# Kernel optimization log

Measured on AMD Instinct MI355X. Metric: run time of the kernel, lower is better.

## Reference

```python
import jax, jax.numpy as jnp
import numpy as np

D_MODEL = 128
N_HEADS = 8
D_K = D_MODEL // N_HEADS
N_NODES = 50000
N_EDGES = 800000


def setup_inputs() -> dict:
    key = jax.random.key(0)
    ks = jax.random.split(key, 8)
    X = jax.random.normal(ks[0], (N_NODES, D_MODEL), dtype=jnp.float32)
    nbr_src = jax.random.randint(ks[1], (N_EDGES,), 0, N_NODES, dtype=jnp.int32)
    nbr_dst = jax.random.randint(ks[2], (N_EDGES,), 0, N_NODES, dtype=jnp.int32)
    s = 1.0 / np.sqrt(D_MODEL)
    W_qkv = jax.random.normal(ks[3], (3 * D_MODEL, D_MODEL), dtype=jnp.float32) * s
    w_bias = jax.random.normal(ks[4], (N_HEADS, D_MODEL), dtype=jnp.float32) * s
    W_gate = jax.random.normal(ks[5], (D_MODEL, D_MODEL), dtype=jnp.float32) * s
    b_gate = jax.random.normal(ks[6], (D_MODEL,), dtype=jnp.float32) * s
    W_o = jax.random.normal(ks[7], (D_MODEL, D_MODEL), dtype=jnp.float32) * s
    return {"X": X, "W_qkv": W_qkv, "w_bias": w_bias, "W_gate": W_gate,
            "b_gate": b_gate, "W_o": W_o, "nbr_src": nbr_src,
            "nbr_dst": nbr_dst, "num_cells": N_NODES}


def segment_softmax(scores, seg, num_segments):
    # scores: [E, H], seg: [E] -> softmax over edges sharing the same seg id
    mx = jax.ops.segment_max(scores, seg, num_segments=num_segments)  # [N, H]
    mx = jnp.where(jnp.isfinite(mx), mx, -1e9)
    exp_s = jnp.exp(scores - mx[seg])
    sm = jax.ops.segment_sum(exp_s, seg, num_segments=num_segments)  # [N, H]
    return exp_s / (sm[seg] + 1e-12)


def reference(X, W_qkv, w_bias, W_gate, b_gate, W_o, nbr_src, nbr_dst, num_cells):
    H, dk = N_HEADS, D_K
    scale = 1.0 / np.sqrt(dk)
    qkv = (X @ W_qkv.T).reshape(-1, 3, H, dk)      # [N, 3, H, dk]
    Q, K, V = qkv[:, 0], qkv[:, 1], qkv[:, 2]
    gate = jax.nn.sigmoid(X @ W_gate.T + b_gate).reshape(-1, H, dk)
    bias = X @ w_bias.T                             # [N, H]
    scores = jnp.einsum('ehd,ehd->eh', Q[nbr_src], K[nbr_dst]) * scale + bias[nbr_src]
    attn = segment_softmax(scores, nbr_src, num_cells)          # [E, H]
    out = jax.ops.segment_sum(attn[:, :, None] * V[nbr_dst], nbr_src,
                              num_segments=num_cells)           # [N, H, dk]
    return (gate * out).reshape(-1, D_MODEL) @ W_o.T
```

## Files before the change

### kernel.cpp

```cpp
#include <hip/hip_runtime.h>
#include <hip/hip_fp16.h>

#define DM 128
#define NHEADS 8
#define MAXDEG 64
#define SROW 136

typedef _Float16 half8 __attribute__((ext_vector_type(8)));
typedef _Float16 half2v __attribute__((ext_vector_type(2)));
typedef float floatx4 __attribute__((ext_vector_type(4)));

union H8 { half8 v; half2v h2[4]; };

__device__ __forceinline__ void prefetch_B(
    int tid, int c, const float* __restrict__ Wqkv,
    const float* __restrict__ Wgate, const float* __restrict__ wbias,
    float4 pf[4][2]) {
#pragma unroll
  for (int i = 0; i < 4; i++) {
    int u = tid + i * 256;
    int r = u >> 4;
    int cc = (u & 15) * 8;
    int grow = c * 64 + r;
    const float* src = nullptr;
    if (grow < 384)      src = Wqkv + (size_t)grow * 128 + cc;
    else if (grow < 512) src = Wgate + (size_t)(grow - 384) * 128 + cc;
    else if (grow < 520) src = wbias + (size_t)(grow - 512) * 128 + cc;
    if (src) {
      pf[i][0] = ((const float4*)src)[0];
      pf[i][1] = ((const float4*)src)[1];
    } else {
      pf[i][0] = make_float4(0.f, 0.f, 0.f, 0.f);
      pf[i][1] = make_float4(0.f, 0.f, 0.f, 0.f);
    }
  }
}

__global__ __launch_bounds__(256) void proj_csr(
    const float* __restrict__ X, const float* __restrict__ Wqkv,
    const float* __restrict__ Wgate, const float* __restrict__ wbias,
    const float* __restrict__ b_gate,
    const int* __restrict__ nsrc, const int* __restrict__ ndst,
    int* __restrict__ cnt, unsigned short* __restrict__ csr_dst,
    _Float16* __restrict__ Q, _Float16* __restrict__ KV,
    _Float16* __restrict__ gate, float* __restrict__ bias,
    int M, int E, int P) {
  __shared__ _Float16 As[128 * SROW];
  __shared__ _Float16 Bs[64 * SROW];
  int tid = threadIdx.x;
  int bid = blockIdx.x;

  if (bid >= P) {
    int ebase = (bid - P) * 8192;
    for (int g = 0; g < 4; g++) {
      int s[8], d[8];
#pragma unroll
      for (int j = 0; j < 8; j++) {
        int e = ebase + (g * 8 + j) * 256 + tid;
        s[j] = (e < E) ? __builtin_nontemporal_load(nsrc + e) : -1;
        d[j] = (e < E) ? __builtin_nontemporal_load(ndst + e) : 0;
      }
#pragma unroll
      for (int j = 0; j < 8; j++) {
        if (s[j] >= 0) {
          int p = atomicAdd(&cnt[s[j]], 1);
          if (p < MAXDEG) csr_dst[(size_t)s[j] * MAXDEG + p] = (unsigned short)d[j];
        }
      }
    }
    return;
  }

  int m0 = bid * 128;

  float4 pf[4][2];
  prefetch_B(tid, 0, Wqkv, Wgate, wbias, pf);

#pragma unroll
  for (int i = 0; i < 4; i++) {
    int u = tid + i * 256;
    int r = u >> 3;
    int cc = (u & 7) * 16;
    int gr = m0 + r;
    float4 f0, f1, f2, f3;
    if (gr < M) {
      const float4* src = (const float4*)(X + (size_t)gr * 128 + cc);
      f0 = src[0]; f1 = src[1]; f2 = src[2]; f3 = src[3];
    } else {
      f0 = f1 = f2 = f3 = make_float4(0.f, 0.f, 0.f, 0.f);
    }
    half8 h0 = {(_Float16)f0.x, (_Float16)f0.y, (_Float16)f0.z, (_Float16)f0.w,
                (_Float16)f1.x, (_Float16)f1.y, (_Float16)f1.z, (_Float16)f1.w};
    half8 h1 = {(_Float16)f2.x, (_Float16)f2.y, (_Float16)f2.z, (_Float16)f2.w,
                (_Float16)f3.x, (_Float16)f3.y, (_Float16)f3.z, (_Float16)f3.w};
    *(half8*)(As + r * SROW + cc) = h0;
    *(half8*)(As + r * SROW + cc + 8) = h1;
  }

  int wid = tid >> 6, lane = tid & 63;
  int quad = lane >> 4, l16 = lane & 15;
  int mw = wid * 32;

  for (int c = 0; c < 9; c++) {
    __syncthreads();
#pragma unroll
    for (int i = 0; i < 4; i++) {
      int u = tid + i * 256;
      int r = u >> 4;
      int cc = (u & 15) * 8;
      half8 h = {(_Float16)pf[i][0].x, (_Float16)pf[i][0].y,
                 (_Float16)pf[i][0].z, (_Float16)pf[i][0].w,
                 (_Float16)pf[i][1].x, (_Float16)pf[i][1].y,
                 (_Float16)pf[i][1].z, (_Float16)pf[i][1].w};
      *(half8*)(Bs + r * SROW + cc) = h;
    }
    if (c < 8) prefetch_B(tid, c + 1, Wqkv, Wgate, wbias, pf);
    __syncthreads();

    floatx4 acc[2][4] = {};
#pragma unroll
    for (int kc = 0; kc < 4; kc++) {
      int ko = kc * 32 + quad * 8;
      half8 a0 = *(const half8*)(As + (mw + l16) * SROW + ko);
      half8 a1 = *(const half8*)(As + (mw + 16 + l16) * SROW + ko);
      half8 b[4];
#pragma unroll
      for (int ni = 0; ni < 4; ni++)
        b[ni] = *(const half8*)(Bs + (ni * 16 + l16) * SROW + ko);
#pragma unroll
      for (int ni = 0; ni < 4; ni++) {
        acc[0][ni] = __builtin_amdgcn_mfma_f32_16x16x32_f16(a0, b[ni], acc[0][ni], 0, 0, 0);
        acc[1][ni] = __builtin_amdgcn_mfma_f32_16x16x32_f16(a1, b[ni], acc[1][ni], 0, 0, 0);
      }
    }

    if (c == 8) {
      if (l16 < 8) {
#pragma unroll
        for (int mi = 0; mi < 2; mi++)
#pragma unroll
          for (int r = 0; r < 4; r++) {
            int row = m0 + mw + mi * 16 + quad * 4 + r;
            if (row < M) bias[(size_t)row * 8 + l16] = acc[mi][0][r];
          }
      }
    } else {
      int reg = c >> 1;
#pragma unroll
      for (int mi = 0; mi < 2; mi++) {
#pragma unroll
        for (int ni = 0; ni < 4; ni++) {
          int colL = (c & 1) * 64 + ni * 16 + l16;
#pragma unroll
          for (int r = 0; r < 4; r++) {
            int row = m0 + mw + mi * 16 + quad * 4 + r;
            if (row >= M) continue;
            float v = acc[mi][ni][r];
            if (reg == 0)      Q[(size_t)row * 128 + colL] = (_Float16)v;
            else if (reg == 1) KV[(size_t)row * 256 + colL] = (_Float16)v;
            else if (reg == 2) KV[(size_t)row * 256 + 128 + colL] = (_Float16)v;
            else gate[(size_t)row * 128 + colL] =
                   (_Float16)(1.0f / (1.0f + __expf(-(v + b_gate[colL]))));
          }
        }
      }
    }
  }
}

__global__ __launch_bounds__(256) void final_gemm_mfma(
    const _Float16* __restrict__ A, const float* __restrict__ Wo,
    float* __restrict__ C, int M) {
  __shared__ _Float16 As[128 * SROW];
  __shared__ _Float16 Bs[64 * SROW];
  int tid = threadIdx.x;
  int m0 = blockIdx.x * 128, n0 = blockIdx.y * 64;
#pragma unroll
  for (int i = 0; i < 8; i++) {
    int u = tid + i * 256;
    int r = u >> 4;
    int cc = (u & 15) * 8;
    int gr = m0 + r;
    int4 val = make_int4(0, 0, 0, 0);
    if (gr < M) val = *(const int4*)(A + (size_t)gr * 128 + cc);
    *(int4*)(As + r * SROW + cc) = val;
  }
#pragma unroll
  for (int i = 0; i < 4; i++) {
    int u = tid + i * 256;
    int r = u >> 4;
    int cc = (u & 15) * 8;
    const float* src = Wo + (size_t)(n0 + r) * 128 + cc;
    float4 f0 = ((const float4*)src)[0];
    float4 f1 = ((const float4*)src)[1];
    half8 h = {(_Float16)f0.x, (_Float16)f0.y, (_Float16)f0.z, (_Float16)f0.w,
               (_Float16)f1.x, (_Float16)f1.y, (_Float16)f1.z, (_Float16)f1.w};
    *(half8*)(Bs + r * SROW + cc) = h;
  }
  __syncthreads();

  int wid = tid >> 6, lane = tid & 63;
  int quad = lane >> 4, l16 = lane & 15;
  int mw = (wid >> 1) * 64;
  int nw = (wid & 1) * 32;

  floatx4 acc[4][2] = {};
#pragma unroll
  for (int kc = 0; kc < 4; kc++) {
    int ko = kc * 32 + quad * 8;
    half8 a[4], b[2];
#pragma unroll
    for (int mi = 0; mi < 4; mi++)
      a[mi] = *(const half8*)(As + (mw + mi * 16 + l16) * SROW + ko);
#pragma unroll
    for (int ni = 0; ni < 2; ni++)
      b[ni] = *(const half8*)(Bs + (nw + ni * 16 + l16) * SROW + ko);
#pragma unroll
    for (int mi = 0; mi < 4; mi++)
#pragma unroll
      for (int ni = 0; ni < 2; ni++)
        acc[mi][ni] = __builtin_amdgcn_mfma_f32_16x16x32_f16(a[mi], b[ni], acc[mi][ni], 0, 0, 0);
  }
#pragma unroll
  for (int mi = 0; mi < 4; mi++) {
#pragma unroll
    for (int ni = 0; ni < 2; ni++) {
      int col = n0 + nw + ni * 16 + l16;
#pragma unroll
      for (int r = 0; r < 4; r++) {
        int row = m0 + mw + mi * 16 + quad * 4 + r;
        if (row >= M) continue;
        C[(size_t)row * 128 + col] = acc[mi][ni][r];
      }
    }
  }
}

__global__ __launch_bounds__(256) void attn_fused(
    const int* __restrict__ cnt, const unsigned short* __restrict__ csr_dst,
    const _Float16* __restrict__ Q, const _Float16* __restrict__ KV,
    const float* __restrict__ bias, const _Float16* __restrict__ gate,
    _Float16* __restrict__ gated, int N) {
  int wave = threadIdx.x >> 6, lane = threadIdx.x & 63;
  int n = blockIdx.x * 4 + wave;
  if (n >= N) return;
  int deg = __builtin_nontemporal_load(cnt + n);
  if (deg > MAXDEG) deg = MAXDEG;
  int qtr = lane >> 4, l16 = lane & 15;
  int ch0 = l16 * 8;

  int dstv = (int)__builtin_nontemporal_load(csr_dst + (size_t)n * MAXDEG + lane);

  H8 qu; qu.v = __builtin_nontemporal_load((const half8*)(Q + (size_t)n * DM + ch0));
  float bias_h = __builtin_nontemporal_load(bias + (size_t)n * NHEADS + (l16 >> 1));

  float acc[8] = {};
  float den = 0.f;
  int iters = (deg + 3) >> 2;

  H8 kb[4], vb[4];
  bool bb[4];
#pragma unroll
  for (int j = 0; j < 4; j++) {
    bb[j] = false;
    kb[j].v = half8{}; vb[j].v = half8{};
    if (j < iters) {
      int e = j * 4 + qtr;
      bb[j] = e < deg;
      int d = __shfl(dstv, e);
      d = bb[j] ? d : 0;
      const _Float16* kvp = KV + (size_t)d * 256 + ch0;
      kb[j].v = *(const half8*)kvp;
      vb[j].v = *(const half8*)(kvp + 128);
    }
  }

  for (int base = 0; base < iters; base += 4) {
#pragma unroll
    for (int j = 0; j < 4; j++) {
      float p = 0.f;
#pragma unroll
      for (int t = 0; t < 4; t++)
        p = __builtin_amdgcn_fdot2(qu.h2[t], kb[j].h2[t], p, false);
      p += __shfl_xor(p, 1);
      float w = __expf(p * 0.25f + bias_h);
      if (!bb[j]) w = 0.f;
      den += w;
#pragma unroll
      for (int t = 0; t < 8; t++) acc[t] = fmaf(w, (float)vb[j].v[t], acc[t]);
      int idx = base + 4 + j;
      bb[j] = false;
      if (idx < iters) {
        int e = idx * 4 + qtr;
        bb[j] = e < deg;
        int d = __shfl(dstv, e);
        d = bb[j] ? d : 0;
        const _Float16* kvp = KV + (size_t)d * 256 + ch0;
        kb[j].v = *(const half8*)kvp;
        vb[j].v = *(const half8*)(kvp + 128);
      }
    }
  }

#pragma unroll
  for (int j = 0; j < 8; j++) acc[j] += __shfl_xor(acc[j], 16);
#pragma unroll
  for (int j = 0; j < 8; j++) acc[j] += __shfl_xor(acc[j], 32);
  den += __shfl_xor(den, 16);
  den += __shfl_xor(den, 32);

  if (qtr == 0) {
    float inv = 1.0f / (den + 1e-12f);
    half8 gv = __builtin_nontemporal_load((const half8*)(gate + (size_t)n * DM + ch0));
    half8 o;
#pragma unroll
    for (int j = 0; j < 8; j++) o[j] = (_Float16)(acc[j] * inv * (float)gv[j]);
    __builtin_nontemporal_store(o, (half8*)(gated + (size_t)n * DM + ch0));
  }
}

extern "C" void kernel_launch(void* const* d_in, const int* in_sizes, int n_in,
                              void* d_out, int out_size, void* d_ws, size_t ws_size,
                              hipStream_t stream) {
  const float* X     = (const float*)d_in[0];
  const float* Wqkv  = (const float*)d_in[1];
  const float* wbias = (const float*)d_in[2];
  const float* Wgate = (const float*)d_in[3];
  const float* bgate = (const float*)d_in[4];
  const float* Wo    = (const float*)d_in[5];
  const int*   nsrc  = (const int*)d_in[6];
  const int*   ndst  = (const int*)d_in[7];
  int N = in_sizes[0] / 128;
  int E = in_sizes[6];
  float* out = (float*)d_out;

  char* p = (char*)d_ws;
  _Float16* Q16     = (_Float16*)p; p += (size_t)N * 128 * sizeof(_Float16);
  _Float16* KV16    = (_Float16*)p; p += (size_t)N * 256 * sizeof(_Float16);
  _Float16* gate16  = (_Float16*)p; p += (size_t)N * 128 * sizeof(_Float16);
  _Float16* gated16 = (_Float16*)p; p += (size_t)N * 128 * sizeof(_Float16);
  float* bias       = (float*)p;    p += (size_t)N * 8 * sizeof(float);
  int* cnt          = (int*)p;      p += (size_t)N * sizeof(int);
  unsigned short* csr_dst = (unsigned short*)p;
  p += (size_t)N * MAXDEG * sizeof(unsigned short);

  hipMemsetAsync(cnt, 0, (size_t)N * sizeof(int), stream);

  int P = (N + 127) / 128;
  int C = (E + 8191) / 8192;
  proj_csr<<<P + C, 256, 0, stream>>>(X, Wqkv, Wgate, wbias, bgate, nsrc, ndst,
                                      cnt, csr_dst, Q16, KV16, gate16, bias, N, E, P);

  attn_fused<<<(N + 3) / 4, 256, 0, stream>>>(cnt, csr_dst, Q16, KV16, bias,
                                              gate16, gated16, N);

  dim3 fg((N + 127) / 128, 2);
  final_gemm_mfma<<<fg, 256, 0, stream>>>(gated16, Wo, out, N);
}
```

Before: 230.8 us.

## Load GEMM operands directly into registers, drop LDS staging in projection

The projection GEMM now loads X and weight fragments straight from global memory into MFMA register operands, removing the shared-memory tiles and the per-chunk __syncthreads. The CSR-build blocks are moved to the front of the grid so the atomics start early, and the projection outputs use nontemporal stores. The trade-off is more scattered global loads (each lane reads 32-byte pieces, and weights are re-read per wave from cache) and higher register pressure from holding the A fragments across all chunks.

New measurement: 282.1 us. 1.22x slower.

```diff
diff --git a/kernel.cpp b/kernel.cpp
--- a/kernel.cpp
+++ b/kernel.cpp
@@ -12,28 +12,9 @@
 
 union H8 { half8 v; half2v h2[4]; };
 
-__device__ __forceinline__ void prefetch_B(
-    int tid, int c, const float* __restrict__ Wqkv,
-    const float* __restrict__ Wgate, const float* __restrict__ wbias,
-    float4 pf[4][2]) {
-#pragma unroll
-  for (int i = 0; i < 4; i++) {
-    int u = tid + i * 256;
-    int r = u >> 4;
-    int cc = (u & 15) * 8;
-    int grow = c * 64 + r;
-    const float* src = nullptr;
-    if (grow < 384)      src = Wqkv + (size_t)grow * 128 + cc;
-    else if (grow < 512) src = Wgate + (size_t)(grow - 384) * 128 + cc;
-    else if (grow < 520) src = wbias + (size_t)(grow - 512) * 128 + cc;
-    if (src) {
-      pf[i][0] = ((const float4*)src)[0];
-      pf[i][1] = ((const float4*)src)[1];
-    } else {
-      pf[i][0] = make_float4(0.f, 0.f, 0.f, 0.f);
-      pf[i][1] = make_float4(0.f, 0.f, 0.f, 0.f);
-    }
-  }
+__device__ __forceinline__ half8 cvt_h8(float4 f0, float4 f1) {
+  return half8{(_Float16)f0.x, (_Float16)f0.y, (_Float16)f0.z, (_Float16)f0.w,
+               (_Float16)f1.x, (_Float16)f1.y, (_Float16)f1.z, (_Float16)f1.w};
 }
 
 __global__ __launch_bounds__(256) void proj_csr(
@@ -44,14 +25,12 @@
     int* __restrict__ cnt, unsigned short* __restrict__ csr_dst,
     _Float16* __restrict__ Q, _Float16* __restrict__ KV,
     _Float16* __restrict__ gate, float* __restrict__ bias,
-    int M, int E, int P) {
-  __shared__ _Float16 As[128 * SROW];
-  __shared__ _Float16 Bs[64 * SROW];
+    int M, int E, int C) {
   int tid = threadIdx.x;
   int bid = blockIdx.x;
 
-  if (bid >= P) {
-    int ebase = (bid - P) * 8192;
+  if (bid < C) {
+    int ebase = bid * 8192;
     for (int g = 0; g < 4; g++) {
       int s[8], d[8];
 #pragma unroll
@@ -71,66 +50,56 @@
     return;
   }
 
-  int m0 = bid * 128;
-
-  float4 pf[4][2];
-  prefetch_B(tid, 0, Wqkv, Wgate, wbias, pf);
-
-#pragma unroll
-  for (int i = 0; i < 4; i++) {
-    int u = tid + i * 256;
-    int r = u >> 3;
-    int cc = (u & 7) * 16;
-    int gr = m0 + r;
-    float4 f0, f1, f2, f3;
-    if (gr < M) {
-      const float4* src = (const float4*)(X + (size_t)gr * 128 + cc);
-      f0 = src[0]; f1 = src[1]; f2 = src[2]; f3 = src[3];
-    } else {
-      f0 = f1 = f2 = f3 = make_float4(0.f, 0.f, 0.f, 0.f);
-    }
-    half8 h0 = {(_Float16)f0.x, (_Float16)f0.y, (_Float16)f0.z, (_Float16)f0.w,
-                (_Float16)f1.x, (_Float16)f1.y, (_Float16)f1.z, (_Float16)f1.w};
-    half8 h1 = {(_Float16)f2.x, (_Float16)f2.y, (_Float16)f2.z, (_Float16)f2.w,
-                (_Float16)f3.x, (_Float16)f3.y, (_Float16)f3.z, (_Float16)f3.w};
-    *(half8*)(As + r * SROW + cc) = h0;
-    *(half8*)(As + r * SROW + cc + 8) = h1;
-  }
-
+  int pbid = bid - C;
+  int m0 = pbid * 128;
   int wid = tid >> 6, lane = tid & 63;
   int quad = lane >> 4, l16 = lane & 15;
   int mw = wid * 32;
-
+  int kb = quad * 8;
+
+  half8 af[2][4];
+#pragma unroll
+  for (int mi = 0; mi < 2; mi++) {
+    int gr = m0 + mw + mi * 16 + l16;
+#pragma unroll
+    for (int kc = 0; kc < 4; kc++) {
+      float4 f0 = make_float4(0.f, 0.f, 0.f, 0.f), f1 = f0;
+      if (gr < M) {
+        const float4* s = (const float4*)(X + (size_t)gr * 128 + kc * 32 + kb);
+        f0 = s[0]; f1 = s[1];
+      }
+      af[mi][kc] = cvt_h8(f0, f1);
+    }
+  }
+
+#pragma unroll
   for (int c = 0; c < 9; c++) {
-    __syncthreads();
-#pragma unroll
-    for (int i = 0; i < 4; i++) {
-      int u = tid + i * 256;
-      int r = u >> 4;
-      int cc = (u & 15) * 8;
-      half8 h = {(_Float16)pf[i][0].x, (_Float16)pf[i][0].y,
-                 (_Float16)pf[i][0].z, (_Float16)pf[i][0].w,
-                 (_Float16)pf[i][1].x, (_Float16)pf[i][1].y,
-                 (_Float16)pf[i][1].z, (_Float16)pf[i][1].w};
-      *(half8*)(Bs + r * SROW + cc) = h;
-    }
-    if (c < 8) prefetch_B(tid, c + 1, Wqkv, Wgate, wbias, pf);
-    __syncthreads();
+    half8 bf[4][4];
+#pragma unroll
+    for (int ni = 0; ni < 4; ni++) {
+      int nr = c * 64 + ni * 16 + l16;
+      const float* src = nullptr;
+      if (nr < 384)      src = Wqkv + (size_t)nr * 128;
+      else if (nr < 512) src = Wgate + (size_t)(nr - 384) * 128;
+      else if (nr < 520) src = wbias + (size_t)(nr - 512) * 128;
+#pragma unroll
+      for (int kc = 0; kc < 4; kc++) {
+        float4 f0 = make_float4(0.f, 0.f, 0.f, 0.f), f1 = f0;
+        if (src) {
+          const float4* s = (const float4*)(src + kc * 32 + kb);
+          f0 = s[0]; f1 = s[1];
+        }
+        bf[ni][kc] = cvt_h8(f0, f1);
+      }
+    }
 
     floatx4 acc[2][4] = {};
 #pragma unroll
     for (int kc = 0; kc < 4; kc++) {
-      int ko = kc * 32 + quad * 8;
-      half8 a0 = *(const half8*)(As + (mw + l16) * SROW + ko);
-      half8 a1 = *(const half8*)(As + (mw + 16 + l16) * SROW + ko);
-      half8 b[4];
-#pragma unroll
-      for (int ni = 0; ni < 4; ni++)
-        b[ni] = *(const half8*)(Bs + (ni * 16 + l16) * SROW + ko);
 #pragma unroll
       for (int ni = 0; ni < 4; ni++) {
-        acc[0][ni] = __builtin_amdgcn_mfma_f32_16x16x32_f16(a0, b[ni], acc[0][ni], 0, 0, 0);
-        acc[1][ni] = __builtin_amdgcn_mfma_f32_16x16x32_f16(a1, b[ni], acc[1][ni], 0, 0, 0);
+        acc[0][ni] = __builtin_amdgcn_mfma_f32_16x16x32_f16(af[0][kc], bf[ni][kc], acc[0][ni], 0, 0, 0);
+        acc[1][ni] = __builtin_amdgcn_mfma_f32_16x16x32_f16(af[1][kc], bf[ni][kc], acc[1][ni], 0, 0, 0);
       }
     }
 
@@ -141,7 +110,8 @@
 #pragma unroll
           for (int r = 0; r < 4; r++) {
             int row = m0 + mw + mi * 16 + quad * 4 + r;
-            if (row < M) bias[(size_t)row * 8 + l16] = acc[mi][0][r];
+            if (row < M)
+              __builtin_nontemporal_store(acc[mi][0][r], bias + (size_t)row * 8 + l16);
           }
       }
     } else {
@@ -156,11 +126,16 @@
             int row = m0 + mw + mi * 16 + quad * 4 + r;
             if (row >= M) continue;
             float v = acc[mi][ni][r];
-            if (reg == 0)      Q[(size_t)row * 128 + colL] = (_Float16)v;
-            else if (reg == 1) KV[(size_t)row * 256 + colL] = (_Float16)v;
-            else if (reg == 2) KV[(size_t)row * 256 + 128 + colL] = (_Float16)v;
-            else gate[(size_t)row * 128 + colL] =
-                   (_Float16)(1.0f / (1.0f + __expf(-(v + b_gate[colL]))));
+            if (reg == 0)
+              __builtin_nontemporal_store((_Float16)v, Q + (size_t)row * 128 + colL);
+            else if (reg == 1)
+              __builtin_nontemporal_store((_Float16)v, KV + (size_t)row * 256 + colL);
+            else if (reg == 2)
+              __builtin_nontemporal_store((_Float16)v, KV + (size_t)row * 256 + 128 + colL);
+            else {
+              _Float16 gv = (_Float16)(1.0f / (1.0f + __expf(-(v + b_gate[colL]))));
+              __builtin_nontemporal_store(gv, gate + (size_t)row * 128 + colL);
+            }
           }
         }
       }
@@ -193,9 +168,7 @@
     const float* src = Wo + (size_t)(n0 + r) * 128 + cc;
     float4 f0 = ((const float4*)src)[0];
     float4 f1 = ((const float4*)src)[1];
-    half8 h = {(_Float16)f0.x, (_Float16)f0.y, (_Float16)f0.z, (_Float16)f0.w,
-               (_Float16)f1.x, (_Float16)f1.y, (_Float16)f1.z, (_Float16)f1.w};
-    *(half8*)(Bs + r * SROW + cc) = h;
+    *(half8*)(Bs + r * SROW + cc) = cvt_h8(f0, f1);
   }
   __syncthreads();
 
@@ -348,8 +321,8 @@
 
   int P = (N + 127) / 128;
   int C = (E + 8191) / 8192;
-  proj_csr<<<P + C, 256, 0, stream>>>(X, Wqkv, Wgate, wbias, bgate, nsrc, ndst,
-                                      cnt, csr_dst, Q16, KV16, gate16, bias, N, E, P);
+  proj_csr<<<C + P, 256, 0, stream>>>(X, Wqkv, Wgate, wbias, bgate, nsrc, ndst,
+                                      cnt, csr_dst, Q16, KV16, gate16, bias, N, E, C);
 
   attn_fused<<<(N + 3) / 4, 256, 0, stream>>>(cnt, csr_dst, Q16, KV16, bias,
                                               gate16, gated16, N);
```

## Halve projection tile rows, drop weight register prefetch, use normal store for gated

Applied to the files above, without the earlier changes.

The projection GEMM now handles 64 rows per block instead of 128. That doubles the block count and halves shared memory and accumulator registers per block, aiming at higher occupancy and better load balance across CUs. The register-level software prefetch of the next weight chunk is removed, so weight loads now sit directly before each barrier, and each weight chunk is re-read and re-converted by twice as many blocks. The gated output store in the attention kernel changes from nontemporal to a normal store so it can stay in cache for the final GEMM.

After: 233.8 us. About the same (+1.3%).

```diff
diff --git a/kernel.cpp b/kernel.cpp
--- a/kernel.cpp
+++ b/kernel.cpp
@@ -12,28 +12,9 @@
 
 union H8 { half8 v; half2v h2[4]; };
 
-__device__ __forceinline__ void prefetch_B(
-    int tid, int c, const float* __restrict__ Wqkv,
-    const float* __restrict__ Wgate, const float* __restrict__ wbias,
-    float4 pf[4][2]) {
-#pragma unroll
-  for (int i = 0; i < 4; i++) {
-    int u = tid + i * 256;
-    int r = u >> 4;
-    int cc = (u & 15) * 8;
-    int grow = c * 64 + r;
-    const float* src = nullptr;
-    if (grow < 384)      src = Wqkv + (size_t)grow * 128 + cc;
-    else if (grow < 512) src = Wgate + (size_t)(grow - 384) * 128 + cc;
-    else if (grow < 520) src = wbias + (size_t)(grow - 512) * 128 + cc;
-    if (src) {
-      pf[i][0] = ((const float4*)src)[0];
-      pf[i][1] = ((const float4*)src)[1];
-    } else {
-      pf[i][0] = make_float4(0.f, 0.f, 0.f, 0.f);
-      pf[i][1] = make_float4(0.f, 0.f, 0.f, 0.f);
-    }
-  }
+__device__ __forceinline__ half8 cvt_h8(float4 f0, float4 f1) {
+  return half8{(_Float16)f0.x, (_Float16)f0.y, (_Float16)f0.z, (_Float16)f0.w,
+               (_Float16)f1.x, (_Float16)f1.y, (_Float16)f1.z, (_Float16)f1.w};
 }
 
 __global__ __launch_bounds__(256) void proj_csr(
@@ -45,7 +26,7 @@
     _Float16* __restrict__ Q, _Float16* __restrict__ KV,
     _Float16* __restrict__ gate, float* __restrict__ bias,
     int M, int E, int P) {
-  __shared__ _Float16 As[128 * SROW];
+  __shared__ _Float16 As[64 * SROW];
   __shared__ _Float16 Bs[64 * SROW];
   int tid = threadIdx.x;
   int bid = blockIdx.x;
@@ -71,13 +52,10 @@
     return;
   }
 
-  int m0 = bid * 128;
-
-  float4 pf[4][2];
-  prefetch_B(tid, 0, Wqkv, Wgate, wbias, pf);
-
-#pragma unroll
-  for (int i = 0; i < 4; i++) {
+  int m0 = bid * 64;
+
+#pragma unroll
+  for (int i = 0; i < 2; i++) {
     int u = tid + i * 256;
     int r = u >> 3;
     int cc = (u & 7) * 16;
@@ -89,17 +67,13 @@
     } else {
       f0 = f1 = f2 = f3 = make_float4(0.f, 0.f, 0.f, 0.f);
     }
-    half8 h0 = {(_Float16)f0.x, (_Float16)f0.y, (_Float16)f0.z, (_Float16)f0.w,
-                (_Float16)f1.x, (_Float16)f1.y, (_Float16)f1.z, (_Float16)f1.w};
-    half8 h1 = {(_Float16)f2.x, (_Float16)f2.y, (_Float16)f2.z, (_Float16)f2.w,
-                (_Float16)f3.x, (_Float16)f3.y, (_Float16)f3.z, (_Float16)f3.w};
-    *(half8*)(As + r * SROW + cc) = h0;
-    *(half8*)(As + r * SROW + cc + 8) = h1;
+    *(half8*)(As + r * SROW + cc) = cvt_h8(f0, f1);
+    *(half8*)(As + r * SROW + cc + 8) = cvt_h8(f2, f3);
   }
 
   int wid = tid >> 6, lane = tid & 63;
   int quad = lane >> 4, l16 = lane & 15;
-  int mw = wid * 32;
+  int mw = wid * 16;
 
   for (int c = 0; c < 9; c++) {
     __syncthreads();
@@ -108,60 +82,58 @@
       int u = tid + i * 256;
       int r = u >> 4;
       int cc = (u & 15) * 8;
-      half8 h = {(_Float16)pf[i][0].x, (_Float16)pf[i][0].y,
-                 (_Float16)pf[i][0].z, (_Float16)pf[i][0].w,
-                 (_Float16)pf[i][1].x, (_Float16)pf[i][1].y,
-                 (_Float16)pf[i][1].z, (_Float16)pf[i][1].w};
+      int grow = c * 64 + r;
+      const float* src = nullptr;
+      if (grow < 384)      src = Wqkv + (size_t)grow * 128 + cc;
+      else if (grow < 512) src = Wgate + (size_t)(grow - 384) * 128 + cc;
+      else if (grow < 520) src = wbias + (size_t)(grow - 512) * 128 + cc;
+      half8 h = {};
+      if (src) {
+        float4 f0 = ((const float4*)src)[0];
+        float4 f1 = ((const float4*)src)[1];
+        h = cvt_h8(f0, f1);
+      }
       *(half8*)(Bs + r * SROW + cc) = h;
     }
-    if (c < 8) prefetch_B(tid, c + 1, Wqkv, Wgate, wbias, pf);
     __syncthreads();
 
-    floatx4 acc[2][4] = {};
+    floatx4 acc[4] = {};
 #pragma unroll
     for (int kc = 0; kc < 4; kc++) {
       int ko = kc * 32 + quad * 8;
       half8 a0 = *(const half8*)(As + (mw + l16) * SROW + ko);
-      half8 a1 = *(const half8*)(As + (mw + 16 + l16) * SROW + ko);
       half8 b[4];
 #pragma unroll
       for (int ni = 0; ni < 4; ni++)
         b[ni] = *(const half8*)(Bs + (ni * 16 + l16) * SROW + ko);
 #pragma unroll
-      for (int ni = 0; ni < 4; ni++) {
-        acc[0][ni] = __builtin_amdgcn_mfma_f32_16x16x32_f16(a0, b[ni], acc[0][ni], 0, 0, 0);
-        acc[1][ni] = __builtin_amdgcn_mfma_f32_16x16x32_f16(a1, b[ni], acc[1][ni], 0, 0, 0);
-      }
+      for (int ni = 0; ni < 4; ni++)
+        acc[ni] = __builtin_amdgcn_mfma_f32_16x16x32_f16(a0, b[ni], acc[ni], 0, 0, 0);
     }
 
     if (c == 8) {
       if (l16 < 8) {
 #pragma unroll
-        for (int mi = 0; mi < 2; mi++)
-#pragma unroll
-          for (int r = 0; r < 4; r++) {
-            int row = m0 + mw + mi * 16 + quad * 4 + r;
-            if (row < M) bias[(size_t)row * 8 + l16] = acc[mi][0][r];
-          }
+        for (int r = 0; r < 4; r++) {
+          int row = m0 + mw + quad * 4 + r;
+          if (row < M) bias[(size_t)row * 8 + l16] = acc[0][r];
+        }
       }
     } else {
       int reg = c >> 1;
 #pragma unroll
-      for (int mi = 0; mi < 2; mi++) {
-#pragma unroll
-        for (int ni = 0; ni < 4; ni++) {
-          int colL = (c & 1) * 64 + ni * 16 + l16;
-#pragma unroll
-          for (int r = 0; r < 4; r++) {
-            int row = m0 + mw + mi * 16 + quad * 4 + r;
-            if (row >= M) continue;
-            float v = acc[mi][ni][r];
-            if (reg == 0)      Q[(size_t)row * 128 + colL] = (_Float16)v;
-            else if (reg == 1) KV[(size_t)row * 256 + colL] = (_Float16)v;
-            else if (reg == 2) KV[(size_t)row * 256 + 128 + colL] = (_Float16)v;
-            else gate[(size_t)row * 128 + colL] =
-                   (_Float16)(1.0f / (1.0f + __expf(-(v + b_gate[colL]))));
-          }
+      for (int ni = 0; ni < 4; ni++) {
+        int colL = (c & 1) * 64 + ni * 16 + l16;
+#pragma unroll
+        for (int r = 0; r < 4; r++) {
+          int row = m0 + mw + quad * 4 + r;
+          if (row >= M) continue;
+          float v = acc[ni][r];
+          if (reg == 0)      Q[(size_t)row * 128 + colL] = (_Float16)v;
+          else if (reg == 1) KV[(size_t)row * 256 + colL] = (_Float16)v;
+          else if (reg == 2) KV[(size_t)row * 256 + 128 + colL] = (_Float16)v;
+          else gate[(size_t)row * 128 + colL] =
+                 (_Float16)(1.0f / (1.0f + __expf(-(v + b_gate[colL]))));
         }
       }
     }
@@ -193,9 +165,7 @@
     const float* src = Wo + (size_t)(n0 + r) * 128 + cc;
     float4 f0 = ((const float4*)src)[0];
     float4 f1 = ((const float4*)src)[1];
-    half8 h = {(_Float16)f0.x, (_Float16)f0.y, (_Float16)f0.z, (_Float16)f0.w,
-               (_Float16)f1.x, (_Float16)f1.y, (_Float16)f1.z, (_Float16)f1.w};
-    *(half8*)(Bs + r * SROW + cc) = h;
+    *(half8*)(Bs + r * SROW + cc) = cvt_h8(f0, f1);
   }
   __syncthreads();
 
@@ -315,7 +285,7 @@
     half8 o;
 #pragma unroll
     for (int j = 0; j < 8; j++) o[j] = (_Float16)(acc[j] * inv * (float)gv[j]);
-    __builtin_nontemporal_store(o, (half8*)(gated + (size_t)n * DM + ch0));
+    *(half8*)(gated + (size_t)n * DM + ch0) = o;
   }
 }
 
@@ -346,7 +316,7 @@
 
   hipMemsetAsync(cnt, 0, (size_t)N * sizeof(int), stream);
 
-  int P = (N + 127) / 128;
+  int P = (N + 63) / 64;
   int C = (E + 8191) / 8192;
   proj_csr<<<P + C, 256, 0, stream>>>(X, Wqkv, Wgate, wbias, bgate, nsrc, ndst,
                                       cnt, csr_dst, Q16, KV16, gate16, bias, N, E, P);
```
